# Kernel tuning notes

Hardware: AMD Instinct MI355X
Metric: run time of the kernel (lower is better)

## Reference

```python
import jax, jax.numpy as jnp
import numpy as np

N = 262144
H = 256
POS_L, DIR_L = 10, 4


def _encode(x, L):
    # classic NeRF sinusoidal encoding with identity: [N,3] -> [N, 3 + 6*L]
    f = 2.0 ** jnp.arange(L, dtype=x.dtype)          # [L]
    xf = x[:, :, None] * f                            # [N,3,L]
    n = x.shape[0]
    return jnp.concatenate([x, jnp.sin(xf).reshape(n, -1), jnp.cos(xf).reshape(n, -1)], axis=1)


def setup_inputs() -> dict:
    key = jax.random.key(0)
    ks = iter(jax.random.split(key, 32))
    inp = {
        "pos": jax.random.normal(next(ks), (N, 3), jnp.float32),
        "dir": jax.random.normal(next(ks), (N, 3), jnp.float32),
        "pixel_width": jax.random.uniform(next(ks), (N, 1), dtype=jnp.float32),
        "t_start": jax.random.uniform(next(ks), (N, 1), dtype=jnp.float32),
        "t_end": jax.random.uniform(next(ks), (N, 1), dtype=jnp.float32),
    }
    pe_dim = 3 + 6 * POS_L   # 63
    de_dim = 3 + 6 * DIR_L   # 27
    dims = {
        "w00": (pe_dim, H), "w01": (H, H), "w02": (H, H), "w03": (H, H),
        "w10": (H + pe_dim, H), "w11": (H, H), "w12": (H, H), "w13": (H, H),
        "cw0": (H + de_dim, H // 2), "cw1": (H // 2, 4),
    }
    for name, (i, o) in dims.items():
        inp[name] = jax.random.normal(next(ks), (i, o), jnp.float32) * (1.0 / np.sqrt(i))
        inp[name.replace("w", "b", 1)] = jnp.zeros((o,), jnp.float32)
    return inp


def _nerf(pos, dir, w00, b00, w01, b01, w02, b02, w03, b03,
          w10, b10, w11, b11, w12, b12, w13, b13, cw0, cb0, cw1, cb1):
    pe = _encode(pos, POS_L)   # [N,63]
    de = _encode(dir, DIR_L)   # [N,27]
    r = jax.nn.relu
    # segment 0 (4 linears, ReLU between all, plus inter-segment ReLU)
    z = r(pe @ w00 + b00)
    z = r(z @ w01 + b01)
    z = r(z @ w02 + b02)
    z = r(z @ w03 + b03)
    # segment 1: positional encoding re-concatenated (skip connection)
    z = jnp.concatenate([z, pe], axis=1)              # [N,319]
    z = r(z @ w10 + b10)
    z = r(z @ w11 + b11)
    z = r(z @ w12 + b12)
    z = z @ w13 + b13                                 # no activation after last segment
    # color head: direction encoding concatenated (delayed_direction=True)
    h = r(jnp.concatenate([z, de], axis=1) @ cw0 + cb0)   # [N,128]
    out = h @ cw1 + cb1                                    # [N,4] (rgb + density, delayed_density=True)
    d = out[:, -1]
    density = jnp.where(d > 8.0, d, jax.nn.softplus(d))    # Softplus(threshold=8)
    rgb = jax.nn.sigmoid(out[:, :3])
    return density, rgb


def reference(pos, dir, pixel_width, t_start, t_end,
              w00, b00, w01, b01, w02, b02, w03, b03,
              w10, b10, w11, b11, w12, b12, w13, b13,
              cw0, cb0, cw1, cb1):
    # pixel_width / t_start / t_end are consumed only by mip-style encoders; the
    # classic sinusoidal encoder used here ignores them (kept for signature parity).
    return _nerf(pos, dir, w00, b00, w01, b01, w02, b02, w03, b03,
                 w10, b10, w11, b11, w12, b12, w13, b13, cw0, cb0, cw1, cb1)
```

## Files before the change

### kernel.cpp

```cpp
#include <hip/hip_runtime.h>
#include <hip/hip_bf16.h>
#include <math.h>

typedef unsigned short u16;
typedef unsigned int   u32;
typedef __bf16 bf16x8 __attribute__((ext_vector_type(8)));
typedef float  f32x4  __attribute__((ext_vector_type(4)));

#define NRAYS 262144
#define NBLK  (NRAYS / 64)

enum : int { PO0=0, PO1=16384, PO2=81920, PO3=147456, PO4=212992,
             PO5=294912, PO6=360448, PO7=425984, PO8=491520, PO9=528384 };
#define TOTAL_PACK_ELEMS 530432

__device__ __forceinline__ u16 f2bf(float x) {
  return (u16)((__float_as_uint(x) + 0x8000u) >> 16);
}

struct PackArgs {
  const float* src[10];
  int K[10]; int N[10]; int l2mt[10]; int cstart[11];
};

__global__ __launch_bounds__(256) void pack_w(PackArgs a, u16* __restrict__ dst)
{
  int e = blockIdx.x * 256 + threadIdx.x;
  if (e >= TOTAL_PACK_ELEMS) return;
  int chunk = e >> 9;
  int li = 0;
  #pragma unroll
  for (int t = 1; t < 10; ++t) li += (chunk >= a.cstart[t]) ? 1 : 0;
  int lc = chunk - a.cstart[li];
  int ks = lc >> a.l2mt[li];
  int mt = lc - (ks << a.l2mt[li]);
  int lane = (e >> 3) & 63, j = e & 7;
  int k = ks * 32 + ((lane >> 4) << 3) + j;
  int n = mt * 16 + (lane & 15);
  float v = 0.f;
  if (k < a.K[li] && n < a.N[li]) v = a.src[li][(size_t)k * a.N[li] + n];
  u32 u = __float_as_uint(v);
  dst[e] = (u16)((u + 0x7FFFu + ((u >> 16) & 1u)) >> 16);
}

template<int MT_W>
__device__ __forceinline__ void binit(f32x4 acc[MT_W][4],
    const float* __restrict__ bias, int chbase, int lane)
{
  const int q = lane >> 4;
  #pragma unroll
  for (int mt = 0; mt < MT_W; ++mt) {
    float4 bv = *(const float4*)(bias + chbase + mt * 16 + q * 4);
    #pragma unroll
    for (int nt = 0; nt < 4; ++nt)
      acc[mt][nt] = (f32x4){bv.x, bv.y, bv.z, bv.w};
  }
}

template<int MT_W, int NSTEPS, int MT_TOTAL, int STRIDE>
__device__ __forceinline__ void gseg(f32x4 acc[MT_W][4],
    const u16* __restrict__ zb, int cbase8,
    const u16* __restrict__ wl, int mt0, int ksbase, int lane)
{
  const int q = lane >> 4, llo = lane & 15;
  #pragma unroll
  for (int ks = 0; ks < NSTEPS; ++ks) {
    int c8s = ((cbase8 + ks * 4 + q) ^ (llo & 7));
    const u16* bp = zb + llo * STRIDE + c8s * 8;
    bf16x8 b[4];
    #pragma unroll
    for (int nt = 0; nt < 4; ++nt)
      b[nt] = *(const bf16x8*)(bp + nt * 16 * STRIDE);
    const u16* wp = wl + ((ksbase + ks) * MT_TOTAL + mt0) * 512 + lane * 8;
    bf16x8 a[MT_W];
    #pragma unroll
    for (int mt = 0; mt < MT_W; ++mt)
      a[mt] = *(const bf16x8*)(wp + mt * 512);
    #pragma unroll
    for (int mt = 0; mt < MT_W; ++mt)
      #pragma unroll
      for (int nt = 0; nt < 4; ++nt)
        acc[mt][nt] = __builtin_amdgcn_mfma_f32_16x16x32_bf16(a[mt], b[nt], acc[mt][nt], 0, 0, 0);
  }
}

template<int MT_W, bool RELU>
__device__ __forceinline__ void zstore(f32x4 acc[MT_W][4],
    int chbase, u16* dst, int lane)
{
  const int llo = lane & 15, q = lane >> 4;
  #pragma unroll
  for (int mt = 0; mt < MT_W; ++mt) {
    int ch = chbase + mt * 16 + q * 4;
    int off0 = (((ch >> 3) ^ (llo & 7)) << 3) + (ch & 7);
    #pragma unroll
    for (int nt = 0; nt < 4; ++nt) {
      f32x4 v = acc[mt][nt];
      float x0 = v.x, x1 = v.y, x2 = v.z, x3 = v.w;
      if (RELU) { x0 = fmaxf(x0, 0.f); x1 = fmaxf(x1, 0.f);
                  x2 = fmaxf(x2, 0.f); x3 = fmaxf(x3, 0.f); }
      u32 a0 = __float_as_uint(x0) + 0x8000u;
      u32 a1 = __float_as_uint(x1) + 0x8000u;
      u32 a2 = __float_as_uint(x2) + 0x8000u;
      u32 a3 = __float_as_uint(x3) + 0x8000u;
      uint2 pk;
      pk.x = (a1 & 0xFFFF0000u) | (a0 >> 16);
      pk.y = (a3 & 0xFFFF0000u) | (a2 >> 16);
      *(uint2*)(dst + (nt * 16 + llo) * 256 + off0) = pk;
    }
  }
}

__device__ __forceinline__ void wr_pe(u16* peb, int r, int c, u16 v) {
  peb[r * 64 + (((c >> 3) ^ (r & 7)) << 3) + (c & 7)];
  peb[r * 64 + (((c >> 3) ^ (r & 7)) << 3) + (c & 7)] = v;
}

__global__ __launch_bounds__(512, 4) void nerf_fused(
    const float* __restrict__ pos,  const float* __restrict__ dirv,
    const float* __restrict__ b00,  const float* __restrict__ b01,
    const float* __restrict__ b02,  const float* __restrict__ b03,
    const float* __restrict__ b10,  const float* __restrict__ b11,
    const float* __restrict__ b12,  const float* __restrict__ b13,
    const float* __restrict__ cb0,  const float* __restrict__ cb1,
    const u16* __restrict__ W, float* __restrict__ out)
{
  __shared__ __align__(16) u16 zA[64 * 256];
  __shared__ __align__(16) u16 zB[64 * 256];
  __shared__ __align__(16) u16 peb[64 * 64];
  float* xyzf = (float*)zB;

  const int tid = threadIdx.x;
  const int rb  = blockIdx.x * 64;
  const int lane = tid & 63, wid = tid >> 6;

  if (tid < 192) {
    int r = tid / 3, c = tid - r * 3;
    xyzf[r * 8 + c] = pos[(size_t)(rb + r) * 3 + c];
  }
  __syncthreads();

  #pragma unroll
  for (int i = tid; i < 64 * 30; i += 512) {
    int r = i / 30, t = i - r * 30;
    int j = t / 10, l = t - j * 10;
    float x = xyzf[r * 8 + j] * (float)(1 << l);
    wr_pe(peb, r, 3 + t,  f2bf(__sinf(x)));
    wr_pe(peb, r, 33 + t, f2bf(__cosf(x)));
  }
  if (tid < 256) {
    int r = tid >> 2, c = tid & 3;
    u16 v = 0; int col = 63;
    if (c < 3) { col = c; v = f2bf(xyzf[r * 8 + c]); }
    wr_pe(peb, r, col, v);
  }
  __syncthreads();

  f32x4 acc[2][4];
  const int mt0 = wid * 2, chb = wid * 32;

  binit<2>(acc, b00, chb, lane);
  gseg<2, 2, 16, 64>(acc, peb, 0, W + PO0, mt0, 0, lane);
  zstore<2, true>(acc, chb, zA, lane);
  __syncthreads();
  binit<2>(acc, b01, chb, lane);
  gseg<2, 8, 16, 256>(acc, zA, 0, W + PO1, mt0, 0, lane);
  zstore<2, true>(acc, chb, zB, lane);
  __syncthreads();
  binit<2>(acc, b02, chb, lane);
  gseg<2, 8, 16, 256>(acc, zB, 0, W + PO2, mt0, 0, lane);
  zstore<2, true>(acc, chb, zA, lane);
  __syncthreads();
  binit<2>(acc, b03, chb, lane);
  gseg<2, 8, 16, 256>(acc, zA, 0, W + PO3, mt0, 0, lane);
  zstore<2, true>(acc, chb, zB, lane);
  __syncthreads();
  binit<2>(acc, b10, chb, lane);
  gseg<2, 8, 16, 256>(acc, zB, 0, W + PO4, mt0, 0, lane);
  gseg<2, 2, 16, 64>(acc, peb, 0, W + PO4, mt0, 8, lane);
  zstore<2, true>(acc, chb, zA, lane);
  __syncthreads();
  #pragma unroll
  for (int i = tid; i < 64 * 16; i += 512) {
    int r = i >> 4, t = i & 15;
    if (t < 12) {
      int j = t >> 2, l = t & 3;
      float x = dirv[(size_t)(rb + r) * 3 + j] * (float)(1 << l);
      wr_pe(peb, r, 32 + 3 + t,  f2bf(__sinf(x)));
      wr_pe(peb, r, 32 + 15 + t, f2bf(__cosf(x)));
    } else {
      wr_pe(peb, r, 32 + 15 + t, 0);
    }
  }
  if (tid < 256) {
    int r = tid >> 2, c = tid & 3;
    u16 v = 0; int col = 31;
    if (c < 3) { col = c; v = f2bf(dirv[(size_t)(rb + r) * 3 + c]); }
    wr_pe(peb, r, 32 + col, v);
  }
  binit<2>(acc, b11, chb, lane);
  gseg<2, 8, 16, 256>(acc, zA, 0, W + PO5, mt0, 0, lane);
  zstore<2, true>(acc, chb, zB, lane);
  __syncthreads();
  binit<2>(acc, b12, chb, lane);
  gseg<2, 8, 16, 256>(acc, zB, 0, W + PO6, mt0, 0, lane);
  zstore<2, true>(acc, chb, zA, lane);
  __syncthreads();
  binit<2>(acc, b13, chb, lane);
  gseg<2, 8, 16, 256>(acc, zA, 0, W + PO7, mt0, 0, lane);
  zstore<2, false>(acc, chb, zB, lane);
  __syncthreads();
  {
    f32x4 acc8[1][4];
    binit<1>(acc8, cb0, wid * 16, lane);
    gseg<1, 8, 8, 256>(acc8, zB, 0, W + PO8, wid, 0, lane);
    gseg<1, 1, 8, 64>(acc8, peb, 4, W + PO8, wid, 8, lane);
    zstore<1, true>(acc8, wid * 16, zA, lane);
    __syncthreads();
  }
  if (wid < 4) {
    const u16* W9 = W + PO9;
    const int q = lane >> 4, llo = lane & 15;
    const int r = wid * 16 + llo;
    f32x4 c9 = (f32x4){0.f, 0.f, 0.f, 0.f};
    #pragma unroll
    for (int ks = 0; ks < 4; ++ks) {
      int c8s = ((ks * 4 + q) ^ (llo & 7));
      bf16x8 b = *(const bf16x8*)(zA + r * 256 + c8s * 8);
      bf16x8 a = *(const bf16x8*)(W9 + ks * 512 + lane * 8);
      c9 = __builtin_amdgcn_mfma_f32_16x16x32_bf16(a, b, c9, 0, 0, 0);
    }
    if (q == 0) {
      int ray = rb + r;
      float o0 = c9.x + cb1[0];
      float o1 = c9.y + cb1[1];
      float o2 = c9.z + cb1[2];
      float dv = c9.w + cb1[3];
      out[ray] = (dv > 8.f) ? dv : log1pf(__expf(dv));
      float* rgb = out + NRAYS + (size_t)ray * 3;
      rgb[0] = 1.f / (1.f + __expf(-o0));
      rgb[1] = 1.f / (1.f + __expf(-o1));
      rgb[2] = 1.f / (1.f + __expf(-o2));
    }
  }
}

extern "C" void kernel_launch(void* const* d_in, const int* in_sizes, int n_in,
                              void* d_out, int out_size, void* d_ws, size_t ws_size,
                              hipStream_t stream)
{
  (void)in_sizes; (void)n_in; (void)out_size; (void)ws_size;
  const float* pos  = (const float*)d_in[0];
  const float* dirv = (const float*)d_in[1];
  PackArgs pa;
  const int widx[10] = {5, 7, 9, 11, 13, 15, 17, 19, 21, 23};
  const int K[10]    = {63, 256, 256, 256, 319, 256, 256, 256, 283, 128};
  const int Nn[10]   = {256, 256, 256, 256, 256, 256, 256, 256, 128, 4};
  const int L2MT[10] = {4, 4, 4, 4, 4, 4, 4, 4, 3, 0};
  const int CS[11]   = {0, 32, 160, 288, 416, 576, 704, 832, 960, 1032, 1036};
  for (int i = 0; i < 10; ++i) {
    pa.src[i] = (const float*)d_in[widx[i]];
    pa.K[i] = K[i]; pa.N[i] = Nn[i]; pa.l2mt[i] = L2MT[i];
  }
  for (int i = 0; i < 11; ++i) pa.cstart[i] = CS[i];

  u16* wp = (u16*)d_ws;
  hipLaunchKernelGGL(pack_w, dim3(TOTAL_PACK_ELEMS / 256), dim3(256), 0, stream, pa, wp);

  hipLaunchKernelGGL(nerf_fused, dim3(NBLK), dim3(512), 0, stream,
      pos, dirv,
      (const float*)d_in[6],  (const float*)d_in[8],
      (const float*)d_in[10], (const float*)d_in[12],
      (const float*)d_in[14], (const float*)d_in[16],
      (const float*)d_in[18], (const float*)d_in[20],
      (const float*)d_in[22], (const float*)d_in[24],
      wp, (float*)d_out);
}
```

Before: 361.3 us.

## Process 128 rays per block with single in-place activation buffer

```diff
diff --git a/kernel.cpp b/kernel.cpp
--- a/kernel.cpp
+++ b/kernel.cpp
@@ -8,7 +8,8 @@
 typedef float  f32x4  __attribute__((ext_vector_type(4)));
 
 #define NRAYS 262144
-#define NBLK  (NRAYS / 64)
+#define RPB   128
+#define NBLK  (NRAYS / RPB)
 
 enum : int { PO0=0, PO1=16384, PO2=81920, PO3=147456, PO4=212992,
              PO5=294912, PO6=360448, PO7=425984, PO8=491520, PO9=528384 };
@@ -59,14 +60,14 @@
 
 template<int MT_W, int NSTEPS, int MT_TOTAL, int STRIDE>
 __device__ __forceinline__ void gseg(f32x4 acc[MT_W][4],
-    const u16* __restrict__ zb, int cbase8,
+    const u16* __restrict__ zb, int rhb, int cbase8,
     const u16* __restrict__ wl, int mt0, int ksbase, int lane)
 {
   const int q = lane >> 4, llo = lane & 15;
   #pragma unroll
   for (int ks = 0; ks < NSTEPS; ++ks) {
     int c8s = ((cbase8 + ks * 4 + q) ^ (llo & 7));
-    const u16* bp = zb + llo * STRIDE + c8s * 8;
+    const u16* bp = zb + (rhb + llo) * STRIDE + c8s * 8;
     bf16x8 b[4];
     #pragma unroll
     for (int nt = 0; nt < 4; ++nt)
@@ -86,7 +87,7 @@
 
 template<int MT_W, bool RELU>
 __device__ __forceinline__ void zstore(f32x4 acc[MT_W][4],
-    int chbase, u16* dst, int lane)
+    int chbase, int rhb, u16* dst, int lane)
 {
   const int llo = lane & 15, q = lane >> 4;
   #pragma unroll
@@ -104,15 +105,14 @@
       u32 a2 = __float_as_uint(x2) + 0x8000u;
       u32 a3 = __float_as_uint(x3) + 0x8000u;
       uint2 pk;
-      pk.x = (a1 & 0xFFFF0000u) | (a0 >> 16);
-      pk.y = (a3 & 0xFFFF0000u) | (a2 >> 16);
-      *(uint2*)(dst + (nt * 16 + llo) * 256 + off0) = pk;
+      pk.x = __builtin_amdgcn_perm(a1, a0, 0x07060302u);
+      pk.y = __builtin_amdgcn_perm(a3, a2, 0x07060302u);
+      *(uint2*)(dst + (rhb + nt * 16 + llo) * 256 + off0) = pk;
     }
   }
 }
 
 __device__ __forceinline__ void wr_pe(u16* peb, int r, int c, u16 v) {
-  peb[r * 64 + (((c >> 3) ^ (r & 7)) << 3) + (c & 7)];
   peb[r * 64 + (((c >> 3) ^ (r & 7)) << 3) + (c & 7)] = v;
 }
 
@@ -125,63 +125,68 @@
     const float* __restrict__ cb0,  const float* __restrict__ cb1,
     const u16* __restrict__ W, float* __restrict__ out)
 {
-  __shared__ __align__(16) u16 zA[64 * 256];
-  __shared__ __align__(16) u16 zB[64 * 256];
-  __shared__ __align__(16) u16 peb[64 * 64];
-  float* xyzf = (float*)zB;
+  __shared__ __align__(16) u16 zb[RPB * 256];
+  __shared__ __align__(16) u16 peb[RPB * 64];
+  float* xyzf = (float*)zb;
 
   const int tid = threadIdx.x;
-  const int rb  = blockIdx.x * 64;
+  const int rb  = blockIdx.x * RPB;
   const int lane = tid & 63, wid = tid >> 6;
 
-  if (tid < 192) {
+  if (tid < 384) {
     int r = tid / 3, c = tid - r * 3;
-    xyzf[r * 8 + c] = pos[(size_t)(rb + r) * 3 + c];
-  }
-  __syncthreads();
-
-  #pragma unroll
-  for (int i = tid; i < 64 * 30; i += 512) {
+    xyzf[r * 4 + c] = pos[(size_t)(rb + r) * 3 + c];
+  }
+  __syncthreads();
+
+  #pragma unroll
+  for (int i = tid; i < RPB * 30; i += 512) {
     int r = i / 30, t = i - r * 30;
     int j = t / 10, l = t - j * 10;
-    float x = xyzf[r * 8 + j] * (float)(1 << l);
+    float x = xyzf[r * 4 + j] * (float)(1 << l);
     wr_pe(peb, r, 3 + t,  f2bf(__sinf(x)));
     wr_pe(peb, r, 33 + t, f2bf(__cosf(x)));
   }
-  if (tid < 256) {
+  {
     int r = tid >> 2, c = tid & 3;
     u16 v = 0; int col = 63;
-    if (c < 3) { col = c; v = f2bf(xyzf[r * 8 + c]); }
+    if (c < 3) { col = c; v = f2bf(xyzf[r * 4 + c]); }
     wr_pe(peb, r, col, v);
   }
   __syncthreads();
 
-  f32x4 acc[2][4];
-  const int mt0 = wid * 2, chb = wid * 32;
-
-  binit<2>(acc, b00, chb, lane);
-  gseg<2, 2, 16, 64>(acc, peb, 0, W + PO0, mt0, 0, lane);
-  zstore<2, true>(acc, chb, zA, lane);
-  __syncthreads();
-  binit<2>(acc, b01, chb, lane);
-  gseg<2, 8, 16, 256>(acc, zA, 0, W + PO1, mt0, 0, lane);
-  zstore<2, true>(acc, chb, zB, lane);
-  __syncthreads();
-  binit<2>(acc, b02, chb, lane);
-  gseg<2, 8, 16, 256>(acc, zB, 0, W + PO2, mt0, 0, lane);
-  zstore<2, true>(acc, chb, zA, lane);
-  __syncthreads();
-  binit<2>(acc, b03, chb, lane);
-  gseg<2, 8, 16, 256>(acc, zA, 0, W + PO3, mt0, 0, lane);
-  zstore<2, true>(acc, chb, zB, lane);
-  __syncthreads();
-  binit<2>(acc, b10, chb, lane);
-  gseg<2, 8, 16, 256>(acc, zB, 0, W + PO4, mt0, 0, lane);
-  gseg<2, 2, 16, 64>(acc, peb, 0, W + PO4, mt0, 8, lane);
-  zstore<2, true>(acc, chb, zA, lane);
-  __syncthreads();
-  #pragma unroll
-  for (int i = tid; i < 64 * 16; i += 512) {
+  f32x4 acc[4][4];
+  const int mt0 = (wid & 3) * 4;
+  const int chb = mt0 * 16;
+  const int rh  = (wid >> 2) * 64;
+
+  binit<4>(acc, b00, chb, lane);
+  gseg<4, 2, 16, 64>(acc, peb, rh, 0, W + PO0, mt0, 0, lane);
+  __syncthreads();
+  zstore<4, true>(acc, chb, rh, zb, lane);
+  __syncthreads();
+  binit<4>(acc, b01, chb, lane);
+  gseg<4, 8, 16, 256>(acc, zb, rh, 0, W + PO1, mt0, 0, lane);
+  __syncthreads();
+  zstore<4, true>(acc, chb, rh, zb, lane);
+  __syncthreads();
+  binit<4>(acc, b02, chb, lane);
+  gseg<4, 8, 16, 256>(acc, zb, rh, 0, W + PO2, mt0, 0, lane);
+  __syncthreads();
+  zstore<4, true>(acc, chb, rh, zb, lane);
+  __syncthreads();
+  binit<4>(acc, b03, chb, lane);
+  gseg<4, 8, 16, 256>(acc, zb, rh, 0, W + PO3, mt0, 0, lane);
+  __syncthreads();
+  zstore<4, true>(acc, chb, rh, zb, lane);
+  __syncthreads();
+  binit<4>(acc, b10, chb, lane);
+  gseg<4, 8, 16, 256>(acc, zb, rh, 0, W + PO4, mt0, 0, lane);
+  gseg<4, 2, 16, 64>(acc, peb, rh, 0, W + PO4, mt0, 8, lane);
+  __syncthreads();
+  zstore<4, true>(acc, chb, rh, zb, lane);
+  #pragma unroll
+  for (int i = tid; i < RPB * 16; i += 512) {
     int r = i >> 4, t = i & 15;
     if (t < 12) {
       int j = t >> 2, l = t & 3;
@@ -192,33 +197,39 @@
       wr_pe(peb, r, 32 + 15 + t, 0);
     }
   }
-  if (tid < 256) {
+  {
     int r = tid >> 2, c = tid & 3;
     u16 v = 0; int col = 31;
     if (c < 3) { col = c; v = f2bf(dirv[(size_t)(rb + r) * 3 + c]); }
     wr_pe(peb, r, 32 + col, v);
   }
-  binit<2>(acc, b11, chb, lane);
-  gseg<2, 8, 16, 256>(acc, zA, 0, W + PO5, mt0, 0, lane);
-  zstore<2, true>(acc, chb, zB, lane);
-  __syncthreads();
-  binit<2>(acc, b12, chb, lane);
-  gseg<2, 8, 16, 256>(acc, zB, 0, W + PO6, mt0, 0, lane);
-  zstore<2, true>(acc, chb, zA, lane);
-  __syncthreads();
-  binit<2>(acc, b13, chb, lane);
-  gseg<2, 8, 16, 256>(acc, zA, 0, W + PO7, mt0, 0, lane);
-  zstore<2, false>(acc, chb, zB, lane);
-  __syncthreads();
-  {
-    f32x4 acc8[1][4];
-    binit<1>(acc8, cb0, wid * 16, lane);
-    gseg<1, 8, 8, 256>(acc8, zB, 0, W + PO8, wid, 0, lane);
-    gseg<1, 1, 8, 64>(acc8, peb, 4, W + PO8, wid, 8, lane);
-    zstore<1, true>(acc8, wid * 16, zA, lane);
+  __syncthreads();
+  binit<4>(acc, b11, chb, lane);
+  gseg<4, 8, 16, 256>(acc, zb, rh, 0, W + PO5, mt0, 0, lane);
+  __syncthreads();
+  zstore<4, true>(acc, chb, rh, zb, lane);
+  __syncthreads();
+  binit<4>(acc, b12, chb, lane);
+  gseg<4, 8, 16, 256>(acc, zb, rh, 0, W + PO6, mt0, 0, lane);
+  __syncthreads();
+  zstore<4, true>(acc, chb, rh, zb, lane);
+  __syncthreads();
+  binit<4>(acc, b13, chb, lane);
+  gseg<4, 8, 16, 256>(acc, zb, rh, 0, W + PO7, mt0, 0, lane);
+  __syncthreads();
+  zstore<4, false>(acc, chb, rh, zb, lane);
+  __syncthreads();
+  {
+    f32x4 acc8[2][4];
+    const int m8 = (wid & 3) * 2;
+    binit<2>(acc8, cb0, m8 * 16, lane);
+    gseg<2, 8, 8, 256>(acc8, zb, rh, 0, W + PO8, m8, 0, lane);
+    gseg<2, 1, 8, 64>(acc8, peb, rh, 4, W + PO8, m8, 8, lane);
     __syncthreads();
-  }
-  if (wid < 4) {
+    zstore<2, true>(acc8, m8 * 16, rh, zb, lane);
+    __syncthreads();
+  }
+  {
     const u16* W9 = W + PO9;
     const int q = lane >> 4, llo = lane & 15;
     const int r = wid * 16 + llo;
@@ -226,7 +237,7 @@
     #pragma unroll
     for (int ks = 0; ks < 4; ++ks) {
       int c8s = ((ks * 4 + q) ^ (llo & 7));
-      bf16x8 b = *(const bf16x8*)(zA + r * 256 + c8s * 8);
+      bf16x8 b = *(const bf16x8*)(zb + r * 256 + c8s * 8);
       bf16x8 a = *(const bf16x8*)(W9 + ks * 512 + lane * 8);
       c9 = __builtin_amdgcn_mfma_f32_16x16x32_bf16(a, b, c9, 0, 0, 0);
     }
```

Measured after the change: 391.3 us. 1.08x slower.
